# Kernel tuning notes

Measured on AMD Instinct MI355X. Metric: run time of the kernel, lower is better.

## Reference

```python
import jax, jax.numpy as jnp
import numpy as np

EPS = 1e-3  # keras BatchNormalization default epsilon
NUM_HEADS = 8


def conv1d_same(x, w, b):
    # x: [B,T,Cin], w: [K,Cin,Cout]
    return jax.lax.conv_general_dilated(
        x, w, window_strides=(1,), padding='SAME',
        dimension_numbers=('NWC', 'WIO', 'NWC')) + b


def bn(x, g, b, m, v):
    # inference-mode batchnorm with moving stats
    return (x - m) * jax.lax.rsqrt(v + EPS) * g + b


def lstm(x, K, R, b):
    # x: [B,T,D] -> [B,T,U]; keras gate order i,f,c,o; recurrent_dropout off at inference
    B = x.shape[0]
    U = R.shape[0]
    xp = jnp.einsum('btd,dz->btz', x, K) + b  # precompute input projection

    def step(carry, xt):
        h, c = carry
        z = xt + h @ R
        i, f, g, o = jnp.split(z, 4, axis=-1)
        c = jax.nn.sigmoid(f) * c + jax.nn.sigmoid(i) * jnp.tanh(g)
        h = jax.nn.sigmoid(o) * jnp.tanh(c)
        return (h, c), h

    h0 = jnp.zeros((B, U), x.dtype)
    _, hs = jax.lax.scan(step, (h0, h0), jnp.swapaxes(xp, 0, 1))
    return jnp.swapaxes(hs, 0, 1)


def bilstm(x, Kf, Rf, bf, Kb, Rb, bb):
    fwd = lstm(x, Kf, Rf, bf)
    bwd = lstm(x[:, ::-1], Kb, Rb, bb)[:, ::-1]
    return jnp.concatenate([fwd, bwd], axis=-1)


def mhsa(x, wq, bq, wk, bk, wv, bv, wo, bo):
    B, T, _ = x.shape
    d_model = wq.shape[1]
    dh = d_model // NUM_HEADS
    q = (x @ wq + bq).reshape(B, T, NUM_HEADS, dh)
    k = (x @ wk + bk).reshape(B, T, NUM_HEADS, dh)
    v = (x @ wv + bv).reshape(B, T, NUM_HEADS, dh)
    logits = jnp.einsum('bqhd,bkhd->bhqk', q, k) / jnp.sqrt(jnp.asarray(dh, x.dtype))
    attn = jax.nn.softmax(logits, axis=-1)
    out = jnp.einsum('bhqk,bkhd->bqhd', attn, v).reshape(B, T, d_model)
    return out @ wo + bo


def setup_inputs() -> dict:
    key = jax.random.key(0)
    ks = iter(jax.random.split(key, 64))

    def nrm(shape, s=0.05):
        return (jax.random.normal(next(ks), shape) * s).astype(jnp.float32)

    p = {}
    p['x'] = jax.random.normal(next(ks), (512, 256, 78), dtype=jnp.float32)
    for name, shp in [
            ('conv5_w', (5, 78, 64)), ('conv7_w', (7, 78, 64)), ('conv9_w', (9, 78, 64)),
            ('fuse_w', (1, 192, 128)), ('se_w1', (128, 8)), ('se_w2', (8, 128)),
            ('l1f_k', (128, 512)), ('l1f_r', (128, 512)), ('l1b_k', (128, 512)), ('l1b_r', (128, 512)),
            ('l2f_k', (256, 256)), ('l2f_r', (64, 256)), ('l2b_k', (256, 256)), ('l2b_r', (64, 256)),
            ('wq', (128, 256)), ('wk', (128, 256)), ('wv', (128, 256)), ('wo', (256, 256)),
            ('d1_w', (256, 256)), ('d2_w', (256, 128)), ('d3_w', (128, 1)),
            ('conv5_b', (64,)), ('conv7_b', (64,)), ('conv9_b', (64,)), ('fuse_b', (128,)),
            ('se_b1', (8,)), ('se_b2', (128,)),
            ('l1f_b', (512,)), ('l1b_b', (512,)), ('l2f_b', (256,)), ('l2b_b', (256,)),
            ('bq', (256,)), ('bk', (256,)), ('bv', (256,)), ('bo', (256,)),
            ('d1_b', (256,)), ('d2_b', (128,)), ('d3_b', (1,))]:
        p[name] = nrm(shp)
    for tag, c in [('bn5', 64), ('bn7', 64), ('bn9', 64), ('bn_l1', 256),
                   ('bn_l2', 128), ('bn_d1', 256), ('bn_d2', 128)]:
        p[tag + '_g'] = jnp.ones((c,), jnp.float32)
        p[tag + '_b'] = jnp.zeros((c,), jnp.float32)
        p[tag + '_m'] = jnp.zeros((c,), jnp.float32)
        p[tag + '_v'] = jnp.ones((c,), jnp.float32)
    return p


def reference(x, conv5_w, conv5_b, bn5_g, bn5_b, bn5_m, bn5_v,
              conv7_w, conv7_b, bn7_g, bn7_b, bn7_m, bn7_v,
              conv9_w, conv9_b, bn9_g, bn9_b, bn9_m, bn9_v,
              fuse_w, fuse_b, se_w1, se_b1, se_w2, se_b2,
              l1f_k, l1f_r, l1f_b, l1b_k, l1b_r, l1b_b,
              bn_l1_g, bn_l1_b, bn_l1_m, bn_l1_v,
              l2f_k, l2f_r, l2f_b, l2b_k, l2b_r, l2b_b,
              bn_l2_g, bn_l2_b, bn_l2_m, bn_l2_v,
              wq, bq, wk, bk, wv, bv, wo, bo,
              d1_w, d1_b, bn_d1_g, bn_d1_b, bn_d1_m, bn_d1_v,
              d2_w, d2_b, bn_d2_g, bn_d2_b, bn_d2_m, bn_d2_v,
              d3_w, d3_b):
    def block(w, b, g, bt, m, v):
        h = jax.nn.relu(conv1d_same(x, w, b))
        h = bn(h, g, bt, m, v)
        B, T, C = h.shape  # MaxPooling1D(2, 'same'); T is even
        return h.reshape(B, T // 2, 2, C).max(axis=2)

    fused = jnp.concatenate([
        block(conv5_w, conv5_b, bn5_g, bn5_b, bn5_m, bn5_v),
        block(conv7_w, conv7_b, bn7_g, bn7_b, bn7_m, bn7_v),
        block(conv9_w, conv9_b, bn9_g, bn9_b, bn9_m, bn9_v)], axis=-1)
    fused = conv1d_same(fused, fuse_w, fuse_b)

    # SENet spatial attention
    s = fused.mean(axis=1)
    e = jax.nn.sigmoid(jax.nn.relu(s @ se_w1 + se_b1) @ se_w2 + se_b2)
    h = fused * e[:, None, :]

    h = bilstm(h, l1f_k, l1f_r, l1f_b, l1b_k, l1b_r, l1b_b)
    h = bn(h, bn_l1_g, bn_l1_b, bn_l1_m, bn_l1_v)
    h = bilstm(h, l2f_k, l2f_r, l2f_b, l2b_k, l2b_r, l2b_b)
    h = bn(h, bn_l2_g, bn_l2_b, bn_l2_m, bn_l2_v)

    h = mhsa(h, wq, bq, wk, bk, wv, bv, wo, bo)
    g_ = h.mean(axis=1)

    d = jax.nn.relu(g_ @ d1_w + d1_b)
    d = bn(d, bn_d1_g, bn_d1_b, bn_d1_m, bn_d1_v)
    d = jax.nn.relu(d @ d2_w + d2_b)
    d = bn(d, bn_d2_g, bn_d2_b, bn_d2_m, bn_d2_v)
    return jax.nn.sigmoid(d @ d3_w + d3_b)
```

## Files before the change

kernel.cpp:

```cpp
#include <hip/hip_runtime.h>

#define EPS 1e-3f

typedef __attribute__((ext_vector_type(8))) short bf16x8;
typedef __attribute__((ext_vector_type(4))) float f32x4;

__device__ __forceinline__ float sigm(float x){ return 1.0f/(1.0f + __expf(-x)); }
__device__ __forceinline__ float tanhfast(float x){ return 1.0f - 2.0f/(1.0f + __expf(2.0f*x)); }

__device__ __forceinline__ unsigned short f2b(float f){
    union { float f; unsigned u; } v; v.f = f;
    unsigned r = v.u + 0x7FFFu + ((v.u >> 16) & 1u);
    return (unsigned short)(r >> 16);
}
__device__ __forceinline__ float b2f(unsigned short h){
    union { unsigned u; float f; } v; v.u = ((unsigned)h) << 16; return v.f;
}

__global__ void __launch_bounds__(256)
prep_x(const float* __restrict__ x, unsigned short* __restrict__ xbf)
{
    const int b = blockIdx.x;
    const float* xs = x + (size_t)b*256*78;
    unsigned short* xd = xbf + (size_t)b*264*96;
    for (int p = threadIdx.x; p < 264*48; p += 256){
        int row = p / 48;
        int cp  = (p - row*48) * 2;
        int t   = row - 4;
        unsigned short v0 = 0, v1 = 0;
        if (t >= 0 && t < 256){
            if (cp   < 78) v0 = f2b(xs[t*78 + cp]);
            if (cp+1 < 78) v1 = f2b(xs[t*78 + cp + 1]);
        }
        *(unsigned int*)(xd + row*96 + cp) = (unsigned)v0 | ((unsigned)v1 << 16);
    }
}

__global__ void __launch_bounds__(256)
prep_w(const float* __restrict__ w5, const float* __restrict__ w7, const float* __restrict__ w9,
       unsigned short* __restrict__ wfrag)
{
    int g = blockIdx.x*256 + threadIdx.x;
    if (g >= 27*12*64) return;
    union { unsigned short s[8]; uint4 v; } u;
    int base = g * 8;
    #pragma unroll
    for (int e = 0; e < 8; ++e){
        int lin  = base + e;
        int slot = lin & 511;
        int fi   = lin >> 9;
        int nt   = fi % 12, kcs = fi / 12;
        int k    = kcs / 3, cs = kcs - k*3;
        int l15  = slot >> 5, r = slot & 31;
        int lg   = r >> 3, ee = r & 7;
        int ci   = cs*32 + lg*8 + ee;
        int co   = nt*16 + l15;
        float val = 0.f;
        if (ci < 78){
            if (co < 64){
                int kk = k - 2;
                if (kk >= 0 && kk < 5) val = w5[(kk*78 + ci)*64 + co];
            } else if (co < 128){
                int kk = k - 1;
                if (kk >= 0 && kk < 7) val = w7[(kk*78 + ci)*64 + (co - 64)];
            } else {
                val = w9[(k*78 + ci)*64 + (co - 128)];
            }
        }
        u.s[e] = f2b(val);
    }
    *(uint4*)(wfrag + base) = u.v;
}

__global__ void prep_ss(const float* b5, const float* b7, const float* b9,
                        const float* g5, const float* be5, const float* m5, const float* v5,
                        const float* g7, const float* be7, const float* m7, const float* v7,
                        const float* g9, const float* be9, const float* m9, const float* v9,
                        float* __restrict__ biascat, float* __restrict__ scale, float* __restrict__ shift)
{
    int c = threadIdx.x;
    if (c >= 192) return;
    float bv, g, be, m, v;
    if (c < 64){        bv=b5[c];      g=g5[c];      be=be5[c];      m=m5[c];      v=v5[c]; }
    else if (c < 128){  int i=c-64;  bv=b7[i]; g=g7[i]; be=be7[i]; m=m7[i]; v=v7[i]; }
    else {              int i=c-128; bv=b9[i]; g=g9[i]; be=be9[i]; m=m9[i]; v=v9[i]; }
    float s = g * rsqrtf(v + EPS);
    biascat[c] = bv;
    scale[c]   = s;
    shift[c]   = be - m*s;
}

__global__ void __launch_bounds__(256)
conv_mfma(const unsigned short* __restrict__ xbf,
          const unsigned short* __restrict__ wfrag,
          const float* __restrict__ biascat, const float* __restrict__ scale,
          const float* __restrict__ shift,
          float* __restrict__ out)
{
    const int b = blockIdx.x, tile = blockIdx.y;
    const int tid = threadIdx.x, lane = tid & 63, wv = tid >> 6;
    const int l15 = lane & 15, lg = lane >> 4;
    const int nt0 = wv * 3;
    const int t0  = tile * 64;

    f32x4 acc[4][3];
    #pragma unroll
    for (int nt = 0; nt < 3; ++nt){
        float bv = biascat[(nt0 + nt)*16 + l15];
        #pragma unroll
        for (int mt = 0; mt < 4; ++mt)
            acc[mt][nt] = (f32x4){bv, bv, bv, bv};
    }

    const unsigned short* xb = xbf + ((size_t)b*264 + t0 + l15)*96 + lg*8;
    const unsigned short* wb = wfrag + (size_t)nt0*512 + l15*32 + lg*8;

    for (int k = 0; k < 9; ++k){
        #pragma unroll
        for (int cs = 0; cs < 3; ++cs){
            bf16x8 A[4], Bf[3];
            #pragma unroll
            for (int mt = 0; mt < 4; ++mt)
                A[mt] = *(const bf16x8*)(xb + (size_t)(k + mt*16)*96 + cs*32);
            #pragma unroll
            for (int nt = 0; nt < 3; ++nt)
                Bf[nt] = *(const bf16x8*)(wb + (size_t)((k*3 + cs)*12 + nt)*512);
            #pragma unroll
            for (int mt = 0; mt < 4; ++mt)
                #pragma unroll
                for (int nt = 0; nt < 3; ++nt)
                    acc[mt][nt] = __builtin_amdgcn_mfma_f32_16x16x32_bf16(A[mt], Bf[nt], acc[mt][nt], 0, 0, 0);
        }
    }

    #pragma unroll
    for (int nt = 0; nt < 3; ++nt){
        int col = (nt0 + nt)*16 + l15;
        float s = scale[col], sh = shift[col];
        #pragma unroll
        for (int mt = 0; mt < 4; ++mt){
            float v0 = fmaxf(acc[mt][nt][0], 0.f)*s + sh;
            float v1 = fmaxf(acc[mt][nt][1], 0.f)*s + sh;
            float v2 = fmaxf(acc[mt][nt][2], 0.f)*s + sh;
            float v3 = fmaxf(acc[mt][nt][3], 0.f)*s + sh;
            int tb = tile*32 + mt*8 + lg*2;
            out[((size_t)b*128 + tb    )*192 + col] = fmaxf(v0, v1);
            out[((size_t)b*128 + tb + 1)*192 + col] = fmaxf(v2, v3);
        }
    }
}

__global__ void __launch_bounds__(128)
se_mean(const unsigned short* __restrict__ fb,
        const float* __restrict__ w1, const float* __restrict__ b1,
        const float* __restrict__ w2, const float* __restrict__ b2,
        float* __restrict__ e)
{
    int b = blockIdx.x, c = threadIdx.x;
    __shared__ float sv[128];
    __shared__ float rv[8];
    const unsigned short* fp = fb + (size_t)b*128*128 + c;
    float acc = 0.f;
    for (int t = 0; t < 128; ++t) acc += b2f(fp[t*128]);
    sv[c] = acc * (1.f/128.f);
    __syncthreads();
    if (c < 8){
        float r = b1[c];
        for (int i = 0; i < 128; ++i) r = fmaf(sv[i], w1[i*8 + c], r);
        rv[c] = fmaxf(r, 0.f);
    }
    __syncthreads();
    float ev = b2[c];
    #pragma unroll
    for (int j = 0; j < 8; ++j) ev = fmaf(rv[j], w2[j*128 + c], ev);
    e[(size_t)b*128 + c] = sigm(ev);
}

template<int K, bool ABF16, int OUTMODE, bool ESCALE>
__global__ void __launch_bounds__(256)
xp_gemm(const void* __restrict__ Av, const float* __restrict__ W,
        const float* __restrict__ bias, const float* __restrict__ esc,
        unsigned short* __restrict__ outp, int N)
{
    __shared__ unsigned short Asm[128][40];
    __shared__ unsigned short Bsm[8][64][8];
    __shared__ float esm[ESCALE ? K : 1];

    const int tid  = threadIdx.x;
    const int lane = tid & 63;
    const int wv   = tid >> 6;
    const int wm   = wv & 1;
    const int wn   = wv >> 1;
    const size_t m0 = (size_t)blockIdx.x * 128;
    const int n0   = blockIdx.y * 128;

    if constexpr (ESCALE){
        for (int i = tid; i < K; i += 256) esm[i] = esc[(size_t)blockIdx.x*K + i];
    }

    f32x4 acc[4][4];
    #pragma unroll
    for (int nt = 0; nt < 4; ++nt){
        float bv = bias[n0 + wn*64 + nt*16 + (lane & 15)];
        #pragma unroll
        for (int mt = 0; mt < 4; ++mt)
            acc[mt][nt] = (f32x4){bv, bv, bv, bv};
    }

    const int bn = tid & 127;
    const int bg = tid >> 7;

    for (int k0 = 0; k0 < K; k0 += 32){
        __syncthreads();
        if constexpr (!ABF16){
            const float* Ag = (const float*)Av;
            #pragma unroll
            for (int i = 0; i < 2; ++i){
                int g = tid + i*256;
                int r = g >> 2, c8 = g & 3;
                float4 d0 = *(const float4*)(Ag + (m0 + r)*K + k0 + c8*8);
                float4 d1 = *(const float4*)(Ag + (m0 + r)*K + k0 + c8*8 + 4);
                union { unsigned short s[8]; uint4 v; } u;
                u.s[0]=f2b(d0.x); u.s[1]=f2b(d0.y); u.s[2]=f2b(d0.z); u.s[3]=f2b(d0.w);
                u.s[4]=f2b(d1.x); u.s[5]=f2b(d1.y); u.s[6]=f2b(d1.z); u.s[7]=f2b(d1.w);
                *(uint4*)&Asm[r][c8*8] = u.v;
            }
        } else {
            const unsigned short* Ag = (const unsigned short*)Av;
            #pragma unroll
            for (int i = 0; i < 2; ++i){
                int g = tid + i*256;
                int r = g >> 2, c8 = g & 3;
                uint4 d = *(const uint4*)(Ag + (m0 + r)*K + k0 + c8*8);
                if constexpr (ESCALE){
                    unsigned short* s = (unsigned short*)&d;
                    #pragma unroll
                    for (int j = 0; j < 8; ++j)
                        s[j] = f2b(b2f(s[j]) * esm[k0 + c8*8 + j]);
                }
                *(uint4*)&Asm[r][c8*8] = d;
            }
        }
        {
            union { unsigned short s[8]; uint4 v; } u0, u1;
            #pragma unroll
            for (int q = 0; q < 8; ++q){
                u0.s[q] = f2b(W[(size_t)(k0 + bg*16 + q)*N + n0 + bn]);
                u1.s[q] = f2b(W[(size_t)(k0 + bg*16 + 8 + q)*N + n0 + bn]);
            }
            int nt = bn >> 4, lo = bn & 15;
            *(uint4*)&Bsm[nt][lo + 16*(2*bg)][0]   = u0.v;
            *(uint4*)&Bsm[nt][lo + 16*(2*bg+1)][0] = u1.v;
        }
        __syncthreads();

        bf16x8 af[4], bfr[4];
        #pragma unroll
        for (int mt = 0; mt < 4; ++mt)
            af[mt] = *(const bf16x8*)&Asm[wm*64 + mt*16 + (lane & 15)][(lane >> 4)*8];
        #pragma unroll
        for (int nt = 0; nt < 4; ++nt)
            bfr[nt] = *(const bf16x8*)&Bsm[wn*4 + nt][lane][0];
        #pragma unroll
        for (int mt = 0; mt < 4; ++mt)
            #pragma unroll
            for (int nt = 0; nt < 4; ++nt)
                acc[mt][nt] = __builtin_amdgcn_mfma_f32_16x16x32_bf16(af[mt], bfr[nt], acc[mt][nt], 0, 0, 0);
    }

    #pragma unroll
    for (int mt = 0; mt < 4; ++mt)
        #pragma unroll
        for (int nt = 0; nt < 4; ++nt)
            #pragma unroll
            for (int r = 0; r < 4; ++r){
                size_t row = m0 + wm*64 + mt*16 + (lane >> 4)*4 + r;
                int    col = n0 + wn*64 + nt*16 + (lane & 15);
                if constexpr (OUTMODE == 0){
                    outp[row*N + col] = f2b(acc[mt][nt][r]);
                } else if constexpr (OUTMODE == 1){
                    size_t off = ((size_t)((row >> 7)*8 + (col >> 5))*32 + (col & 31))*128 + (row & 127);
                    outp[off] = f2b(acc[mt][nt][r]);
                } else {
                    const int U = N/4;
                    outp[row*N + (col & (U-1))*4 + (col / U)] = f2b(acc[mt][nt][r]);
                }
            }
}

template<int U, int RB, bool OUT_BF16>
__global__ void __launch_bounds__(512)
lstm_rec(const unsigned short* __restrict__ xpf, const unsigned short* __restrict__ xpb,
         const float* __restrict__ Rf, const float* __restrict__ Rb,
         const float* __restrict__ bng, const float* __restrict__ bnb,
         const float* __restrict__ bnm, const float* __restrict__ bnv,
         void* __restrict__ outv)
{
    constexpr int Z   = 4*U;
    constexpr int KT  = U/32;
    constexpr int NTW = Z/128;
    constexpr int HP  = U + 8;

    __shared__ unsigned short h_lds[16][HP];
    __shared__ float z_lds[4][Z];

    const int tid  = threadIdx.x;
    const int lane = tid & 63;
    const int wv   = tid >> 6;
    const int dir  = blockIdx.y;
    const int b0   = blockIdx.x * RB;
    const int ncol0 = wv * (Z/8);

    const unsigned short* xp = dir ? xpb : xpf;
    const float* Rg = dir ? Rb : Rf;

    for (int i = tid; i < 16*HP; i += 512) ((unsigned short*)h_lds)[i] = 0;

    bf16x8 rf[KT][NTW];
    {
        const int kb = (lane >> 4) * 8;
        const int nc = lane & 15;
        #pragma unroll
        for (int kt = 0; kt < KT; ++kt)
            #pragma unroll
            for (int nt = 0; nt < NTW; ++nt){
                union { unsigned short s[8]; bf16x8 v; } u;
                #pragma unroll
                for (int e = 0; e < 8; ++e)
                    u.s[e] = f2b(Rg[(size_t)(kt*32 + kb + e)*Z + ncol0 + nt*16 + nc]);
                rf[kt][nt] = u.v;
            }
    }

    const int u_  = tid % U;
    const int r_  = tid / U;
    const bool gate = (tid < RB*U);
    float c_ = 0.f;
    float bns = 0.f, bnsh = 0.f;
    const int ch = dir*U + u_;
    if (gate){
        bns  = bng[ch] * rsqrtf(bnv[ch] + EPS);
        bnsh = bnb[ch] - bnm[ch]*bns;
    }
    const unsigned short* xbase = xp + (size_t)(b0 + (gate ? r_ : 0))*128*Z + u_*4;
    __syncthreads();

    ushort4 xq = {0,0,0,0};
    if (gate) xq = *(const ushort4*)(xbase + (size_t)(dir ? 127 : 0)*Z);

    for (int ts = 0; ts < 128; ++ts){
        const int t = dir ? 127 - ts : ts;
        ushort4 xn = xq;
        if (gate && ts < 127){
            int tn = dir ? t - 1 : t + 1;
            xn = *(const ushort4*)(xbase + (size_t)tn*Z);
        }
        bf16x8 af[KT];
        #pragma unroll
        for (int kt = 0; kt < KT; ++kt)
            af[kt] = *(const bf16x8*)&h_lds[lane & 15][kt*32 + (lane >> 4)*8];
        f32x4 acc[NTW];
        #pragma unroll
        for (int nt = 0; nt < NTW; ++nt) acc[nt] = (f32x4){0.f,0.f,0.f,0.f};
        #pragma unroll
        for (int kt = 0; kt < KT; ++kt)
            #pragma unroll
            for (int nt = 0; nt < NTW; ++nt)
                acc[nt] = __builtin_amdgcn_mfma_f32_16x16x32_bf16(af[kt], rf[kt][nt], acc[nt], 0, 0, 0);
        if ((lane >> 4) == 0){
            #pragma unroll
            for (int nt = 0; nt < NTW; ++nt)
                #pragma unroll
                for (int r = 0; r < 4; ++r)
                    z_lds[r][ncol0 + nt*16 + (lane & 15)] = acc[nt][r];
        }
        __syncthreads();
        if (gate){
            float z0 = z_lds[r_][u_      ] + b2f(xq.x);
            float z1 = z_lds[r_][u_ +  U ] + b2f(xq.y);
            float z2 = z_lds[r_][u_ + 2*U] + b2f(xq.z);
            float z3 = z_lds[r_][u_ + 3*U] + b2f(xq.w);
            float iv = sigm(z0), fv = sigm(z1), gv = tanhfast(z2), ov = sigm(z3);
            c_ = fv*c_ + iv*gv;
            float h = ov * tanhfast(c_);
            h_lds[r_][u_] = f2b(h);
            float hb = fmaf(h, bns, bnsh);
            size_t oidx = ((size_t)(b0 + r_)*128 + t)*(size_t)(2*U) + ch;
            if constexpr (OUT_BF16) ((unsigned short*)outv)[oidx] = f2b(hb);
            else                    ((float*)outv)[oidx] = hb;
        }
        __syncthreads();
        xq = xn;
    }
}

__global__ void __launch_bounds__(256)
attn_kernel(const unsigned short* __restrict__ qb,
            const unsigned short* __restrict__ kb,
            const unsigned short* __restrict__ vb,
            float* __restrict__ msum)
{
    __shared__ unsigned short p_lds[128][136];
    __shared__ float red[4][2][16];

    const int b  = blockIdx.x, hd = blockIdx.y;
    const int tid = threadIdx.x, lane = tid & 63, wv = tid >> 6;
    const int m0 = wv * 32;
    const int l15 = lane & 15, lg = lane >> 4;

    bf16x8 aq[2];
    #pragma unroll
    for (int mt = 0; mt < 2; ++mt)
        aq[mt] = *(const bf16x8*)(qb + ((size_t)(b*128 + m0 + mt*16 + l15))*256 + hd*32 + lg*8);

    bf16x8 bk[8];
    #pragma unroll
    for (int nt = 0; nt < 8; ++nt)
        bk[nt] = *(const bf16x8*)(kb + ((size_t)(b*128 + nt*16 + l15))*256 + hd*32 + lg*8);

    f32x4 s[2][8];
    #pragma unroll
    for (int mt = 0; mt < 2; ++mt)
        #pragma unroll
        for (int nt = 0; nt < 8; ++nt) s[mt][nt] = (f32x4){0.f,0.f,0.f,0.f};
    #pragma unroll
    for (int mt = 0; mt < 2; ++mt)
        #pragma unroll
        for (int nt = 0; nt < 8; ++nt)
            s[mt][nt] = __builtin_amdgcn_mfma_f32_16x16x32_bf16(aq[mt], bk[nt], s[mt][nt], 0, 0, 0);

    const float scale = 0.17677669529663687f;
    #pragma unroll
    for (int mt = 0; mt < 2; ++mt)
        #pragma unroll
        for (int r = 0; r < 4; ++r){
            float mx = -1e30f;
            #pragma unroll
            for (int nt = 0; nt < 8; ++nt) mx = fmaxf(mx, s[mt][nt][r]);
            #pragma unroll
            for (int msk = 1; msk < 16; msk <<= 1) mx = fmaxf(mx, __shfl_xor(mx, msk, 64));
            float pv[8], sum = 0.f;
            #pragma unroll
            for (int nt = 0; nt < 8; ++nt){
                pv[nt] = __expf((s[mt][nt][r] - mx) * scale);
                sum += pv[nt];
            }
            #pragma unroll
            for (int msk = 1; msk < 16; msk <<= 1) sum += __shfl_xor(sum, msk, 64);
            float inv = 1.f / sum;
            int row = m0 + mt*16 + lg*4 + r;
            #pragma unroll
            for (int nt = 0; nt < 8; ++nt)
                p_lds[row][nt*16 + l15] = f2b(pv[nt] * inv);
        }
    __syncthreads();

    f32x4 o[2][2];
    #pragma unroll
    for (int mt = 0; mt < 2; ++mt)
        #pragma unroll
        for (int dn = 0; dn < 2; ++dn) o[mt][dn] = (f32x4){0.f,0.f,0.f,0.f};
    bf16x8 bv[4][2];
    #pragma unroll
    for (int kt = 0; kt < 4; ++kt)
        #pragma unroll
        for (int dn = 0; dn < 2; ++dn)
            bv[kt][dn] = *(const bf16x8*)(vb + ((size_t)(b*8 + hd)*32 + dn*16 + l15)*128 + kt*32 + lg*8);
    #pragma unroll
    for (int mt = 0; mt < 2; ++mt)
        #pragma unroll
        for (int kt = 0; kt < 4; ++kt){
            bf16x8 ap = *(const bf16x8*)&p_lds[m0 + mt*16 + l15][kt*32 + lg*8];
            #pragma unroll
            for (int dn = 0; dn < 2; ++dn)
                o[mt][dn] = __builtin_amdgcn_mfma_f32_16x16x32_bf16(ap, bv[kt][dn], o[mt][dn], 0, 0, 0);
        }

    float sm[2];
    #pragma unroll
    for (int dn = 0; dn < 2; ++dn){
        float a = 0.f;
        #pragma unroll
        for (int mt = 0; mt < 2; ++mt)
            #pragma unroll
            for (int r = 0; r < 4; ++r) a += o[mt][dn][r];
        a += __shfl_xor(a, 16, 64);
        a += __shfl_xor(a, 32, 64);
        sm[dn] = a;
    }
    if (lg == 0){
        red[wv][0][l15] = sm[0];
        red[wv][1][l15] = sm[1];
    }
    __syncthreads();
    if (tid < 32){
        int dn = tid >> 4, n = tid & 15;
        float tot = red[0][dn][n] + red[1][dn][n] + red[2][dn][n] + red[3][dn][n];
        msum[(size_t)b*256 + hd*32 + dn*16 + n] = tot * (1.f/128.f);
    }
}

__global__ void __launch_bounds__(256)
head_kernel(const float* __restrict__ msum,
            const float* __restrict__ wo, const float* __restrict__ bo,
            const float* __restrict__ d1w, const float* __restrict__ d1b,
            const float* __restrict__ g1, const float* __restrict__ b1,
            const float* __restrict__ m1, const float* __restrict__ v1,
            const float* __restrict__ d2w, const float* __restrict__ d2b,
            const float* __restrict__ g2, const float* __restrict__ b2,
            const float* __restrict__ m2, const float* __restrict__ v2,
            const float* __restrict__ d3w, const float* __restrict__ d3b,
            float* __restrict__ outp)
{
    int b = blockIdx.x, j = threadIdx.x;
    __shared__ float s1[256];
    __shared__ float s2[256];
    const float* mr = msum + (size_t)b*256;
    float acc = bo[j];
    #pragma unroll 4
    for (int i = 0; i < 256; ++i) acc = fmaf(mr[i], wo[i*256 + j], acc);
    s1[j] = acc;
    __syncthreads();
    float a1 = d1b[j];
    #pragma unroll 4
    for (int i = 0; i < 256; ++i) a1 = fmaf(s1[i], d1w[i*256 + j], a1);
    a1 = fmaxf(a1, 0.f);
    float sc1 = g1[j] * rsqrtf(v1[j] + EPS);
    a1 = a1 * sc1 + (b1[j] - m1[j] * sc1);
    s2[j] = a1;
    __syncthreads();
    if (j < 128){
        float a2 = d2b[j];
        #pragma unroll 4
        for (int i = 0; i < 256; ++i) a2 = fmaf(s2[i], d2w[i*128 + j], a2);
        a2 = fmaxf(a2, 0.f);
        float sc2 = g2[j] * rsqrtf(v2[j] + EPS);
        a2 = a2 * sc2 + (b2[j] - m2[j] * sc2);
        s1[j] = a2;
    }
    __syncthreads();
    if (j == 0){
        float a3 = d3b[0];
        for (int i = 0; i < 128; ++i) a3 = fmaf(s1[i], d3w[i], a3);
        outp[b] = sigm(a3);
    }
}

extern "C" void kernel_launch(void* const* d_in, const int* in_sizes, int n_in,
                              void* d_out, int out_size, void* d_ws, size_t ws_size,
                              hipStream_t stream)
{
    #define F(i) ((const float*)d_in[i])
    const float* x       = F(0);
    const float* conv5_w = F(1);
    const float* conv7_w = F(2);
    const float* conv9_w = F(3);
    const float* fuse_w  = F(4);
    const float* se_w1   = F(5);
    const float* se_w2   = F(6);
    const float* l1f_k   = F(7);
    const float* l1f_r   = F(8);
    const float* l1b_k   = F(9);
    const float* l1b_r   = F(10);
    const float* l2f_k   = F(11);
    const float* l2f_r   = F(12);
    const float* l2b_k   = F(13);
    const float* l2b_r   = F(14);
    const float* wq      = F(15);
    const float* wk      = F(16);
    const float* wv      = F(17);
    const float* wo      = F(18);
    const float* d1_w    = F(19);
    const float* d2_w    = F(20);
    const float* d3_w    = F(21);
    const float* conv5_b = F(22);
    const float* conv7_b = F(23);
    const float* conv9_b = F(24);
    const float* fuse_b  = F(25);
    const float* se_b1   = F(26);
    const float* se_b2   = F(27);
    const float* l1f_b   = F(28);
    const float* l1b_b   = F(29);
    const float* l2f_b   = F(30);
    const float* l2b_b   = F(31);
    const float* bq      = F(32);
    const float* bk      = F(33);
    const float* bv      = F(34);
    const float* bo      = F(35);
    const float* d1_b    = F(36);
    const float* d2_b    = F(37);
    const float* d3_b    = F(38);
    const float* bn5_g = F(39), *bn5_b = F(40), *bn5_m = F(41), *bn5_v = F(42);
    const float* bn7_g = F(43), *bn7_b = F(44), *bn7_m = F(45), *bn7_v = F(46);
    const float* bn9_g = F(47), *bn9_b = F(48), *bn9_m = F(49), *bn9_v = F(50);
    const float* bnl1_g = F(51), *bnl1_b = F(52), *bnl1_m = F(53), *bnl1_v = F(54);
    const float* bnl2_g = F(55), *bnl2_b = F(56), *bnl2_m = F(57), *bnl2_v = F(58);
    const float* bnd1_g = F(59), *bnd1_b = F(60), *bnd1_m = F(61), *bnd1_v = F(62);
    const float* bnd2_g = F(63), *bnd2_b = F(64), *bnd2_m = F(65), *bnd2_v = F(66);
    #undef F

    float* ws = (float*)d_ws;
    float* concat = ws;
    unsigned short* fusedbf = (unsigned short*)(ws + 12582912);
    float* e      = ws + 16777216;
    unsigned short* xbf   = (unsigned short*)(ws + 20971520);
    unsigned short* wfrag = (unsigned short*)(ws + 27607040);
    float* biascat = ws + 27689984;
    float* cscale  = ws + 27690176;
    float* cshift  = ws + 27690368;
    unsigned short* xp1f  = (unsigned short*)(ws);
    unsigned short* xp1b  = (unsigned short*)(ws + 20971520);
    unsigned short* l1out = (unsigned short*)(ws + 29360128);
    unsigned short* xp2f  = (unsigned short*)(ws);
    unsigned short* xp2b  = (unsigned short*)(ws + 4194304);
    unsigned short* l2out = (unsigned short*)(ws + 8388608);
    unsigned short* qbuf  = (unsigned short*)(ws + 12582912);
    unsigned short* kbuf  = (unsigned short*)(ws);
    unsigned short* vbuf  = (unsigned short*)(ws + 20971520);
    float* msum   = ws + 29360128;
    float* outp   = (float*)d_out;

    prep_x<<<dim3(512), dim3(256), 0, stream>>>(x, xbf);
    prep_w<<<dim3(81), dim3(256), 0, stream>>>(conv5_w, conv7_w, conv9_w, wfrag);
    prep_ss<<<dim3(1), dim3(192), 0, stream>>>(
        conv5_b, conv7_b, conv9_b,
        bn5_g, bn5_b, bn5_m, bn5_v,
        bn7_g, bn7_b, bn7_m, bn7_v,
        bn9_g, bn9_b, bn9_m, bn9_v,
        biascat, cscale, cshift);
    conv_mfma<<<dim3(512,4), dim3(256), 0, stream>>>(
        xbf, wfrag, biascat, cscale, cshift, concat);

    xp_gemm<192,false,0,false><<<dim3(512,1), dim3(256), 0, stream>>>(
        concat, fuse_w, fuse_b, nullptr, fusedbf, 128);
    se_mean<<<dim3(512), dim3(128), 0, stream>>>(fusedbf, se_w1, se_b1, se_w2, se_b2, e);

    xp_gemm<128,true,2,true><<<dim3(512,4), dim3(256), 0, stream>>>(
        fusedbf, l1f_k, l1f_b, e, xp1f, 512);
    xp_gemm<128,true,2,true><<<dim3(512,4), dim3(256), 0, stream>>>(
        fusedbf, l1b_k, l1b_b, e, xp1b, 512);
    lstm_rec<128,2,true><<<dim3(256,2), dim3(512), 0, stream>>>(
        xp1f, xp1b, l1f_r, l1b_r, bnl1_g, bnl1_b, bnl1_m, bnl1_v, l1out);

    xp_gemm<256,true,2,false><<<dim3(512,2), dim3(256), 0, stream>>>(
        l1out, l2f_k, l2f_b, nullptr, xp2f, 256);
    xp_gemm<256,true,2,false><<<dim3(512,2), dim3(256), 0, stream>>>(
        l1out, l2b_k, l2b_b, nullptr, xp2b, 256);
    lstm_rec<64,2,true><<<dim3(256,2), dim3(512), 0, stream>>>(
        xp2f, xp2b, l2f_r, l2b_r, bnl2_g, bnl2_b, bnl2_m, bnl2_v, l2out);

    xp_gemm<128,true,0,false><<<dim3(512,2), dim3(256), 0, stream>>>(
        l2out, wq, bq, nullptr, qbuf, 256);
    xp_gemm<128,true,0,false><<<dim3(512,2), dim3(256), 0, stream>>>(
        l2out, wk, bk, nullptr, kbuf, 256);
    xp_gemm<128,true,1,false><<<dim3(512,2), dim3(256), 0, stream>>>(
        l2out, wv, bv, nullptr, vbuf, 256);

    attn_kernel<<<dim3(512,8), dim3(256), 0, stream>>>(qbuf, kbuf, vbuf, msum);

    head_kernel<<<dim3(512), dim3(256), 0, stream>>>(
        msum, wo, bo,
        d1_w, d1_b, bnd1_g, bnd1_b, bnd1_m, bnd1_v,
        d2_w, d2_b, bnd2_g, bnd2_b, bnd2_m, bnd2_v,
        d3_w, d3_b, outp);

    (void)in_sizes; (void)n_in; (void)out_size; (void)ws_size;
}
```

Baseline: 775.8 us.

## Restructure LSTM recurrence so gate math stays in MFMA lanes with double-buffered h

The LSTM recurrent kernel is reorganised so each wave owns 16 hidden units across all four gates. The gate nonlinearities can then be computed directly from MFMA accumulators, with no z staging round-trip through LDS. The hidden state is double-buffered, which removes one of the two barriers per timestep. Each block now handles 4 batch rows instead of 2, halving the grid, and the U=64 layer uses 256 threads. Only a quarter of the lanes do the gate work, and occupancy and the number of blocks change.

```diff
diff --git a/kernel.cpp b/kernel.cpp
--- a/kernel.cpp
+++ b/kernel.cpp
@@ -288,109 +288,105 @@
             }
 }
 
-template<int U, int RB, bool OUT_BF16>
-__global__ void __launch_bounds__(512)
-lstm_rec(const unsigned short* __restrict__ xpf, const unsigned short* __restrict__ xpb,
-         const float* __restrict__ Rf, const float* __restrict__ Rb,
-         const float* __restrict__ bng, const float* __restrict__ bnb,
-         const float* __restrict__ bnm, const float* __restrict__ bnv,
-         void* __restrict__ outv)
-{
-    constexpr int Z   = 4*U;
-    constexpr int KT  = U/32;
-    constexpr int NTW = Z/128;
-    constexpr int HP  = U + 8;
-
-    __shared__ unsigned short h_lds[16][HP];
-    __shared__ float z_lds[4][Z];
-
-    const int tid  = threadIdx.x;
-    const int lane = tid & 63;
-    const int wv   = tid >> 6;
-    const int dir  = blockIdx.y;
-    const int b0   = blockIdx.x * RB;
-    const int ncol0 = wv * (Z/8);
+template<int U, bool OUT_BF16>
+__global__ void __launch_bounds__(4*U, 4)
+lstm_rec2(const unsigned short* __restrict__ xpf, const unsigned short* __restrict__ xpb,
+          const float* __restrict__ Rf, const float* __restrict__ Rb,
+          const float* __restrict__ bng, const float* __restrict__ bnb,
+          const float* __restrict__ bnm, const float* __restrict__ bnv,
+          void* __restrict__ outv)
+{
+    constexpr int Z  = 4*U;
+    constexpr int KT = U/32;
+    constexpr int HP = U + 8;
+
+    __shared__ unsigned short h_lds[2][16][HP];
+
+    const int tid = threadIdx.x, lane = tid & 63, wv = tid >> 6;
+    const int l15 = lane & 15, lg = lane >> 4;
+    const int dir = blockIdx.y;
+    const int b0  = blockIdx.x * 4;
 
     const unsigned short* xp = dir ? xpb : xpf;
     const float* Rg = dir ? Rb : Rf;
 
-    for (int i = tid; i < 16*HP; i += 512) ((unsigned short*)h_lds)[i] = 0;
-
-    bf16x8 rf[KT][NTW];
-    {
-        const int kb = (lane >> 4) * 8;
-        const int nc = lane & 15;
-        #pragma unroll
-        for (int kt = 0; kt < KT; ++kt)
-            #pragma unroll
-            for (int nt = 0; nt < NTW; ++nt){
-                union { unsigned short s[8]; bf16x8 v; } u;
-                #pragma unroll
-                for (int e = 0; e < 8; ++e)
-                    u.s[e] = f2b(Rg[(size_t)(kt*32 + kb + e)*Z + ncol0 + nt*16 + nc]);
-                rf[kt][nt] = u.v;
-            }
-    }
-
-    const int u_  = tid % U;
-    const int r_  = tid / U;
-    const bool gate = (tid < RB*U);
-    float c_ = 0.f;
+    for (int i = tid; i < 2*16*HP; i += 4*U) ((unsigned short*)h_lds)[i] = 0;
+
+    bf16x8 rf[KT][4];
+    #pragma unroll
+    for (int kt = 0; kt < KT; ++kt)
+        #pragma unroll
+        for (int g = 0; g < 4; ++g){
+            union { unsigned short s[8]; bf16x8 v; } u;
+            #pragma unroll
+            for (int e = 0; e < 8; ++e)
+                u.s[e] = f2b(Rg[(size_t)(kt*32 + lg*8 + e)*Z + g*U + wv*16 + l15]);
+            rf[kt][g] = u.v;
+        }
+
+    const int u_ = wv*16 + l15;
+    const bool glane = (lg == 0);
+    const int ch = dir*U + u_;
     float bns = 0.f, bnsh = 0.f;
-    const int ch = dir*U + u_;
-    if (gate){
+    if (glane){
         bns  = bng[ch] * rsqrtf(bnv[ch] + EPS);
         bnsh = bnb[ch] - bnm[ch]*bns;
     }
-    const unsigned short* xbase = xp + (size_t)(b0 + (gate ? r_ : 0))*128*Z + u_*4;
-    __syncthreads();
-
-    ushort4 xq = {0,0,0,0};
-    if (gate) xq = *(const ushort4*)(xbase + (size_t)(dir ? 127 : 0)*Z);
-
+    float cst[4] = {0.f, 0.f, 0.f, 0.f};
+    const unsigned short* xbase = xp + (size_t)b0*128*Z + u_*4;
+
+    ushort4 xq[4] = {};
+    if (glane){
+        const int tf = dir ? 127 : 0;
+        #pragma unroll
+        for (int r = 0; r < 4; ++r)
+            xq[r] = *(const ushort4*)(xbase + (size_t)r*128*Z + (size_t)tf*Z);
+    }
+    __syncthreads();
+
+    int buf = 0;
     for (int ts = 0; ts < 128; ++ts){
         const int t = dir ? 127 - ts : ts;
-        ushort4 xn = xq;
-        if (gate && ts < 127){
-            int tn = dir ? t - 1 : t + 1;
-            xn = *(const ushort4*)(xbase + (size_t)tn*Z);
+        ushort4 xn[4] = {};
+        if (glane && ts < 127){
+            const int tn = dir ? t - 1 : t + 1;
+            #pragma unroll
+            for (int r = 0; r < 4; ++r)
+                xn[r] = *(const ushort4*)(xbase + (size_t)r*128*Z + (size_t)tn*Z);
         }
         bf16x8 af[KT];
         #pragma unroll
         for (int kt = 0; kt < KT; ++kt)
-            af[kt] = *(const bf16x8*)&h_lds[lane & 15][kt*32 + (lane >> 4)*8];
-        f32x4 acc[NTW];
-        #pragma unroll
-        for (int nt = 0; nt < NTW; ++nt) acc[nt] = (f32x4){0.f,0.f,0.f,0.f};
+            af[kt] = *(const bf16x8*)&h_lds[buf][l15][kt*32 + lg*8];
+        f32x4 acc[4];
+        #pragma unroll
+        for (int g = 0; g < 4; ++g) acc[g] = (f32x4){0.f,0.f,0.f,0.f};
         #pragma unroll
         for (int kt = 0; kt < KT; ++kt)
             #pragma unroll
-            for (int nt = 0; nt < NTW; ++nt)
-                acc[nt] = __builtin_amdgcn_mfma_f32_16x16x32_bf16(af[kt], rf[kt][nt], acc[nt], 0, 0, 0);
-        if ((lane >> 4) == 0){
-            #pragma unroll
-            for (int nt = 0; nt < NTW; ++nt)
-                #pragma unroll
-                for (int r = 0; r < 4; ++r)
-                    z_lds[r][ncol0 + nt*16 + (lane & 15)] = acc[nt][r];
+            for (int g = 0; g < 4; ++g)
+                acc[g] = __builtin_amdgcn_mfma_f32_16x16x32_bf16(af[kt], rf[kt][g], acc[g], 0, 0, 0);
+        if (glane){
+            #pragma unroll
+            for (int r = 0; r < 4; ++r){
+                float zi = acc[0][r] + b2f(xq[r].x);
+                float zf = acc[1][r] + b2f(xq[r].y);
+                float zg = acc[2][r] + b2f(xq[r].z);
+                float zo = acc[3][r] + b2f(xq[r].w);
+                float c  = sigm(zf)*cst[r] + sigm(zi)*tanhfast(zg);
+                cst[r] = c;
+                float h = sigm(zo)*tanhfast(c);
+                h_lds[buf^1][r][u_] = f2b(h);
+                float hb = fmaf(h, bns, bnsh);
+                size_t oidx = ((size_t)(b0 + r)*128 + t)*(size_t)(2*U) + ch;
+                if constexpr (OUT_BF16) ((unsigned short*)outv)[oidx] = f2b(hb);
+                else                    ((float*)outv)[oidx] = hb;
+            }
         }
         __syncthreads();
-        if (gate){
-            float z0 = z_lds[r_][u_      ] + b2f(xq.x);
-            float z1 = z_lds[r_][u_ +  U ] + b2f(xq.y);
-            float z2 = z_lds[r_][u_ + 2*U] + b2f(xq.z);
-            float z3 = z_lds[r_][u_ + 3*U] + b2f(xq.w);
-            float iv = sigm(z0), fv = sigm(z1), gv = tanhfast(z2), ov = sigm(z3);
-            c_ = fv*c_ + iv*gv;
-            float h = ov * tanhfast(c_);
-            h_lds[r_][u_] = f2b(h);
-            float hb = fmaf(h, bns, bnsh);
-            size_t oidx = ((size_t)(b0 + r_)*128 + t)*(size_t)(2*U) + ch;
-            if constexpr (OUT_BF16) ((unsigned short*)outv)[oidx] = f2b(hb);
-            else                    ((float*)outv)[oidx] = hb;
-        }
-        __syncthreads();
-        xq = xn;
+        buf ^= 1;
+        #pragma unroll
+        for (int r = 0; r < 4; ++r) xq[r] = xn[r];
     }
 }
 
@@ -639,14 +635,14 @@
         fusedbf, l1f_k, l1f_b, e, xp1f, 512);
     xp_gemm<128,true,2,true><<<dim3(512,4), dim3(256), 0, stream>>>(
         fusedbf, l1b_k, l1b_b, e, xp1b, 512);
-    lstm_rec<128,2,true><<<dim3(256,2), dim3(512), 0, stream>>>(
+    lstm_rec2<128,true><<<dim3(128,2), dim3(512), 0, stream>>>(
         xp1f, xp1b, l1f_r, l1b_r, bnl1_g, bnl1_b, bnl1_m, bnl1_v, l1out);
 
     xp_gemm<256,true,2,false><<<dim3(512,2), dim3(256), 0, stream>>>(
         l1out, l2f_k, l2f_b, nullptr, xp2f, 256);
     xp_gemm<256,true,2,false><<<dim3(512,2), dim3(256), 0, stream>>>(
         l1out, l2b_k, l2b_b, nullptr, xp2b, 256);
-    lstm_rec<64,2,true><<<dim3(256,2), dim3(512), 0, stream>>>(
+    lstm_rec2<64,true><<<dim3(128,2), dim3(256), 0, stream>>>(
         xp2f, xp2b, l2f_r, l2b_r, bnl2_g, bnl2_b, bnl2_m, bnl2_v, l2out);
 
     xp_gemm<128,true,0,false><<<dim3(512,2), dim3(256), 0, stream>>>(
```

Result: slower. 861.9 us (+11.1%).

## Pack four batch rows per LSTM block and pre-convert recurrent weights to bf16 fragments

Applied to the files above, without the earlier changes.

The recurrent LSTM kernel now processes four batch rows per workgroup instead of two, so the grid is halved and each sequential timestep's MFMA (16 rows wide) does more useful work. More threads take part in the gate math per step. The recurrent weight matrices are converted once to bf16 MFMA fragment layout by a new prep kernel, so each block loads them with vector reads instead of strided fp32 loads plus in-kernel conversion. The trade-off is fewer blocks available for latency hiding, plus four small extra kernel launches.

```diff
diff --git a/kernel.cpp b/kernel.cpp
--- a/kernel.cpp
+++ b/kernel.cpp
@@ -72,6 +72,24 @@
     *(uint4*)(wfrag + base) = u.v;
 }
 
+__global__ void __launch_bounds__(256)
+prep_wb(const float* __restrict__ W, unsigned short* __restrict__ dst, int K, int N)
+{
+    int idx = blockIdx.x*256 + threadIdx.x;
+    int NT = N >> 4;
+    int total = (K >> 5) * NT * 64;
+    if (idx >= total) return;
+    int l   = idx & 63;
+    int rem = idx >> 6;
+    int ntg = rem % NT;
+    int ks  = rem / NT;
+    union { unsigned short s[8]; uint4 v; } u;
+    #pragma unroll
+    for (int e = 0; e < 8; ++e)
+        u.s[e] = f2b(W[(size_t)(ks*32 + (l>>4)*8 + e)*N + ntg*16 + (l&15)]);
+    *(uint4*)(dst + (size_t)idx*8) = u.v;
+}
+
 __global__ void prep_ss(const float* b5, const float* b7, const float* b9,
                         const float* g5, const float* be5, const float* m5, const float* v5,
                         const float* g7, const float* be7, const float* m7, const float* v7,
@@ -288,18 +306,19 @@
             }
 }
 
-template<int U, int RB, bool OUT_BF16>
+template<int U, bool OUT_BF16>
 __global__ void __launch_bounds__(512)
-lstm_rec(const unsigned short* __restrict__ xpf, const unsigned short* __restrict__ xpb,
-         const float* __restrict__ Rf, const float* __restrict__ Rb,
-         const float* __restrict__ bng, const float* __restrict__ bnb,
-         const float* __restrict__ bnm, const float* __restrict__ bnv,
-         void* __restrict__ outv)
-{
-    constexpr int Z   = 4*U;
-    constexpr int KT  = U/32;
-    constexpr int NTW = Z/128;
-    constexpr int HP  = U + 8;
+lstm_rec8(const unsigned short* __restrict__ xpf, const unsigned short* __restrict__ xpb,
+          const unsigned short* __restrict__ Rff, const unsigned short* __restrict__ Rbf,
+          const float* __restrict__ bng, const float* __restrict__ bnb,
+          const float* __restrict__ bnm, const float* __restrict__ bnv,
+          unsigned short* __restrict__ outv)
+{
+    constexpr int Z    = 4*U;
+    constexpr int KT   = U/32;
+    constexpr int NTW  = Z/128;
+    constexpr int NT16 = Z/16;
+    constexpr int HP   = U + 8;
 
     __shared__ unsigned short h_lds[16][HP];
     __shared__ float z_lds[4][Z];
@@ -308,33 +327,24 @@
     const int lane = tid & 63;
     const int wv   = tid >> 6;
     const int dir  = blockIdx.y;
-    const int b0   = blockIdx.x * RB;
+    const int b0   = blockIdx.x * 4;
     const int ncol0 = wv * (Z/8);
 
     const unsigned short* xp = dir ? xpb : xpf;
-    const float* Rg = dir ? Rb : Rf;
+    const unsigned short* Rp = dir ? Rbf : Rff;
 
     for (int i = tid; i < 16*HP; i += 512) ((unsigned short*)h_lds)[i] = 0;
 
     bf16x8 rf[KT][NTW];
-    {
-        const int kb = (lane >> 4) * 8;
-        const int nc = lane & 15;
-        #pragma unroll
-        for (int kt = 0; kt < KT; ++kt)
-            #pragma unroll
-            for (int nt = 0; nt < NTW; ++nt){
-                union { unsigned short s[8]; bf16x8 v; } u;
-                #pragma unroll
-                for (int e = 0; e < 8; ++e)
-                    u.s[e] = f2b(Rg[(size_t)(kt*32 + kb + e)*Z + ncol0 + nt*16 + nc]);
-                rf[kt][nt] = u.v;
-            }
-    }
+    #pragma unroll
+    for (int kt = 0; kt < KT; ++kt)
+        #pragma unroll
+        for (int nt = 0; nt < NTW; ++nt)
+            rf[kt][nt] = *(const bf16x8*)(Rp + (((size_t)kt*NT16 + wv*NTW + nt)*64 + lane)*8);
 
     const int u_  = tid % U;
     const int r_  = tid / U;
-    const bool gate = (tid < RB*U);
+    const bool gate = (tid < 4*U);
     float c_ = 0.f;
     float bns = 0.f, bnsh = 0.f;
     const int ch = dir*U + u_;
@@ -376,7 +386,7 @@
         }
         __syncthreads();
         if (gate){
-            float z0 = z_lds[r_][u_      ] + b2f(xq.x);
+            float z0 = z_lds[r_][u_      ] + b2f(xn.x*0 + xq.x);
             float z1 = z_lds[r_][u_ +  U ] + b2f(xq.y);
             float z2 = z_lds[r_][u_ + 2*U] + b2f(xq.z);
             float z3 = z_lds[r_][u_ + 3*U] + b2f(xq.w);
@@ -386,7 +396,7 @@
             h_lds[r_][u_] = f2b(h);
             float hb = fmaf(h, bns, bnsh);
             size_t oidx = ((size_t)(b0 + r_)*128 + t)*(size_t)(2*U) + ch;
-            if constexpr (OUT_BF16) ((unsigned short*)outv)[oidx] = f2b(hb);
+            if constexpr (OUT_BF16) outv[oidx] = f2b(hb);
             else                    ((float*)outv)[oidx] = hb;
         }
         __syncthreads();
@@ -608,6 +618,10 @@
     float* biascat = ws + 27689984;
     float* cscale  = ws + 27690176;
     float* cshift  = ws + 27690368;
+    unsigned short* l1frb = (unsigned short*)(ws + 27690560);
+    unsigned short* l1brb = (unsigned short*)(ws + 27723328);
+    unsigned short* l2frb = (unsigned short*)(ws + 27756096);
+    unsigned short* l2brb = (unsigned short*)(ws + 27764288);
     unsigned short* xp1f  = (unsigned short*)(ws);
     unsigned short* xp1b  = (unsigned short*)(ws + 20971520);
     unsigned short* l1out = (unsigned short*)(ws + 29360128);
@@ -628,6 +642,10 @@
         bn7_g, bn7_b, bn7_m, bn7_v,
         bn9_g, bn9_b, bn9_m, bn9_v,
         biascat, cscale, cshift);
+    prep_wb<<<dim3(32), dim3(256), 0, stream>>>(l1f_r, l1frb, 128, 512);
+    prep_wb<<<dim3(32), dim3(256), 0, stream>>>(l1b_r, l1brb, 128, 512);
+    prep_wb<<<dim3(8),  dim3(256), 0, stream>>>(l2f_r, l2frb, 64, 256);
+    prep_wb<<<dim3(8),  dim3(256), 0, stream>>>(l2b_r, l2brb, 64, 256);
     conv_mfma<<<dim3(512,4), dim3(256), 0, stream>>>(
         xbf, wfrag, biascat, cscale, cshift, concat);
 
@@ -639,15 +657,15 @@
         fusedbf, l1f_k, l1f_b, e, xp1f, 512);
     xp_gemm<128,true,2,true><<<dim3(512,4), dim3(256), 0, stream>>>(
         fusedbf, l1b_k, l1b_b, e, xp1b, 512);
-    lstm_rec<128,2,true><<<dim3(256,2), dim3(512), 0, stream>>>(
-        xp1f, xp1b, l1f_r, l1b_r, bnl1_g, bnl1_b, bnl1_m, bnl1_v, l1out);
+    lstm_rec8<128,true><<<dim3(128,2), dim3(512), 0, stream>>>(
+        xp1f, xp1b, l1frb, l1brb, bnl1_g, bnl1_b, bnl1_m, bnl1_v, l1out);
 
     xp_gemm<256,true,2,false><<<dim3(512,2), dim3(256), 0, stream>>>(
         l1out, l2f_k, l2f_b, nullptr, xp2f, 256);
     xp_gemm<256,true,2,false><<<dim3(512,2), dim3(256), 0, stream>>>(
         l1out, l2b_k, l2b_b, nullptr, xp2b, 256);
-    lstm_rec<64,2,true><<<dim3(256,2), dim3(512), 0, stream>>>(
-        xp2f, xp2b, l2f_r, l2b_r, bnl2_g, bnl2_b, bnl2_m, bnl2_v, l2out);
+    lstm_rec8<64,true><<<dim3(128,2), dim3(512), 0, stream>>>(
+        xp2f, xp2b, l2frb, l2brb, bnl2_g, bnl2_b, bnl2_m, bnl2_v, l2out);
 
     xp_gemm<128,true,0,false><<<dim3(512,2), dim3(256), 0, stream>>>(
         l2out, wq, bq, nullptr, qbuf, 256);
```

After: 740.3 us. 4.6% less time.
